# Performance work log

Hardware: AMD Instinct MI355X
Metric: run time of the kernel (lower is better)

Reference implementation:

```python
import jax, jax.numpy as jnp
from jax import lax
import numpy as np

N, W, H, C = 32, 64, 64, 256
D_STYLE = 256


def setup_inputs() -> dict:
    key = jax.random.key(0)
    k1, k2, k3, k4 = jax.random.split(key, 4)
    inputs = jax.random.normal(k1, (N, W, H, C), dtype=jnp.float32)
    style_coding = jax.random.normal(k2, (N, D_STYLE), dtype=jnp.float32)
    # he_normal-ish init scaling for the learned weights
    w_dense = jax.random.normal(k3, (D_STYLE, C), dtype=jnp.float32) * np.sqrt(2.0 / D_STYLE)
    w_conv = jax.random.normal(k4, (1, 1, C, C), dtype=jnp.float32) * np.sqrt(2.0 / C)
    return {"inputs": inputs, "style_coding": style_coding, "w_dense": w_dense, "w_conv": w_conv}


def reference(inputs, style_coding, w_dense, w_conv):
    # inputs: [N,W,H,C] (NHWC), style_coding: [N,D_style]
    c = inputs.shape[-1]
    scale = 1.0 / jnp.sqrt(jnp.float32(c))
    # Dense(fout_dim, use_bias=False, activation=LeakyReLU())  (keras default alpha=0.3)
    q = jax.nn.leaky_relu(style_coding @ w_dense, negative_slope=0.3)  # [N,C]
    # channel-wise attention: einsum('nwhc,nwhc->nc') with q broadcast over w,h
    ca_logits = jnp.einsum('nwhc,nc->nc', inputs, q) * scale           # [N,C]
    ca = jax.nn.softmax(ca_logits, axis=-1)[:, None, None, :]          # [N,1,1,C]
    # position-wise attention: einsum('nwhc,nwhc->nwh'), softmax over flattened W*H
    pa_logits = jnp.einsum('nwhc,nc->nwh', inputs, q) * scale          # [N,W,H]
    n, w, h = pa_logits.shape
    pa = jax.nn.softmax(pa_logits.reshape(n, w * h), axis=1).reshape(n, w, h, 1)
    x = inputs * ca * pa                                               # [N,W,H,C]
    # DarknetConv2D_BN_Leaky with no norm kwarg: 1x1 conv (no bias) + LeakyReLU(0.1)
    y = lax.conv_general_dilated(x, w_conv, window_strides=(1, 1), padding='SAME',
                                 dimension_numbers=('NHWC', 'HWIO', 'NHWC'))
    return jax.nn.leaky_relu(y, negative_slope=0.1)
```

## Files before the change

kernel.cpp:

```cpp
#include <hip/hip_runtime.h>


#define NBATCH 32
#define PIX 4096
#define CH 256
#define SCALE 0.0625f

typedef __attribute__((ext_vector_type(8))) short short8;
typedef __attribute__((ext_vector_type(4))) short short4v;
typedef __attribute__((ext_vector_type(4))) float floatx4;

__device__ __forceinline__ short f2bf(float x) {
    unsigned u = __builtin_bit_cast(unsigned, x);
    u += 0x7fffu + ((u >> 16) & 1u);
    return (short)(u >> 16);
}

__device__ __forceinline__ void gll16(const void* g, void* l) {
    __builtin_amdgcn_global_load_lds(
        (const __attribute__((address_space(1))) unsigned int*)g,
        (__attribute__((address_space(3))) unsigned int*)l, 16, 0, 0);
}

__global__ __launch_bounds__(256) void style_kernel(
    const float* __restrict__ style, const float* __restrict__ wd,
    float* __restrict__ q)
{
    __shared__ float s[256];
    const int n = blockIdx.x, t = threadIdx.x;
    s[t] = style[n * 256 + t];
    __syncthreads();
    float acc = 0.f;
#pragma unroll 8
    for (int k = 0; k < 256; ++k) acc += s[k] * wd[k * 256 + t];
    q[n * 256 + t] = acc > 0.f ? acc : 0.3f * acc;
}

__global__ __launch_bounds__(256) void reduce_cast_kernel(
    const float* __restrict__ inp, const float* __restrict__ q,
    float* __restrict__ colsum_part, float* __restrict__ pa_logits,
    short* __restrict__ bf16in)
{
    const int n = blockIdx.y;
    const int chunk = blockIdx.x;
    const int lane = threadIdx.x & 63, w = threadIdx.x >> 6;
    const float4 qv = *(const float4*)&q[n * 256 + lane * 4];
    float4 cs = make_float4(0.f, 0.f, 0.f, 0.f);
    const int pbase = chunk * 128 + w * 32;
    const float* base = inp + ((size_t)n * PIX + pbase) * CH;
    short* obase = bf16in + ((size_t)n * PIX + pbase) * CH;
    for (int j = 0; j < 32; ++j) {
        float4 v = *(const float4*)&base[(size_t)j * CH + lane * 4];
        float d = v.x * qv.x + v.y * qv.y + v.z * qv.z + v.w * qv.w;
        cs.x += v.x; cs.y += v.y; cs.z += v.z; cs.w += v.w;
        short4v sv;
        sv.x = f2bf(v.x); sv.y = f2bf(v.y); sv.z = f2bf(v.z); sv.w = f2bf(v.w);
        *(short4v*)&obase[(size_t)j * CH + lane * 4] = sv;
#pragma unroll
        for (int off = 32; off; off >>= 1) d += __shfl_xor(d, off);
        if (lane == 0) pa_logits[n * PIX + pbase + j] = d * SCALE;
    }
    *(float4*)&colsum_part[((size_t)n * 128 + chunk * 4 + w) * 256 + lane * 4] = cs;
}

__global__ __launch_bounds__(256) void softmax_kernel(
    const float* __restrict__ colsum_part, const float* __restrict__ q,
    const float* __restrict__ pa_logits,
    float* __restrict__ ca, float* __restrict__ pa)
{
    __shared__ float red[256];
    const int n = blockIdx.x, t = threadIdx.x;

    float csum = 0.f;
#pragma unroll 8
    for (int i = 0; i < 128; ++i) csum += colsum_part[((size_t)n * 128 + i) * 256 + t];
    float lg = csum * q[n * 256 + t] * SCALE;
    red[t] = lg; __syncthreads();
    for (int s = 128; s > 0; s >>= 1) {
        if (t < s) red[t] = fmaxf(red[t], red[t + s]);
        __syncthreads();
    }
    float m = red[0]; __syncthreads();
    float e = expf(lg - m);
    red[t] = e; __syncthreads();
    for (int s = 128; s > 0; s >>= 1) {
        if (t < s) red[t] += red[t + s];
        __syncthreads();
    }
    ca[n * 256 + t] = e / red[0];
    __syncthreads();

    float lv[16];
    float lmax = -1e30f;
#pragma unroll
    for (int i = 0; i < 16; ++i) {
        lv[i] = pa_logits[n * PIX + t + 256 * i];
        lmax = fmaxf(lmax, lv[i]);
    }
    red[t] = lmax; __syncthreads();
    for (int s = 128; s > 0; s >>= 1) {
        if (t < s) red[t] = fmaxf(red[t], red[t + s]);
        __syncthreads();
    }
    float M = red[0]; __syncthreads();
    float ev[16], lsum = 0.f;
#pragma unroll
    for (int i = 0; i < 16; ++i) { ev[i] = expf(lv[i] - M); lsum += ev[i]; }
    red[t] = lsum; __syncthreads();
    for (int s = 128; s > 0; s >>= 1) {
        if (t < s) red[t] += red[t + s];
        __syncthreads();
    }
    float inv = 1.0f / red[0];
#pragma unroll
    for (int i = 0; i < 16; ++i) pa[n * PIX + t + 256 * i] = ev[i] * inv;
}

__global__ void wscale_kernel(const float* __restrict__ wc,
                              const float* __restrict__ ca,
                              short* __restrict__ wscaled)
{
    __shared__ float tile[32][33];
    const int n = blockIdx.z;
    const int co0 = blockIdx.x * 32, ci0 = blockIdx.y * 32;
    const int tx = threadIdx.x, ty = threadIdx.y;
#pragma unroll
    for (int r = 0; r < 4; ++r)
        tile[ty + r * 8][tx] = wc[(ci0 + ty + r * 8) * 256 + co0 + tx];
    const float cav = ca[n * 256 + ci0 + tx];
    __syncthreads();
#pragma unroll
    for (int r = 0; r < 4; ++r)
        wscaled[(size_t)n * 65536 + (co0 + ty + r * 8) * 256 + ci0 + tx] =
            f2bf(tile[tx][ty + r * 8] * cav);
}

__global__ __launch_bounds__(256, 4) void conv_mfma(
    const short* __restrict__ bf16in, const short* __restrict__ wscaled,
    const float* __restrict__ pa, float* __restrict__ out)
{
    __shared__ __attribute__((aligned(16))) short As[64 * 64];
    __shared__ __attribute__((aligned(16))) short Bs[256 * 64];

    const int n  = blockIdx.y;
    const int m0 = blockIdx.x * 64;
    const int tid = threadIdx.x;
    const int lane = tid & 63, wid = tid >> 6;
    const int l16 = lane & 15, quad = lane >> 4;
    const int l8r = lane >> 3, slot = lane & 7;

    floatx4 acc[4][4] = {};

    const short* Agb = bf16in + ((size_t)n * PIX + m0) * CH;
    const short* Bgb = wscaled + (size_t)n * 65536;

    for (int kb = 0; kb < 4; ++kb) {
        const int k0 = kb * 64;
        if (kb) __syncthreads();
#pragma unroll
        for (int i = 0; i < 2; ++i) {
            const int r = wid * 16 + i * 8 + l8r;
            gll16(Agb + (size_t)r * CH + k0 + ((slot ^ (r & 7)) << 3),
                  &As[(wid * 16 + i * 8) * 64]);
        }
#pragma unroll
        for (int i = 0; i < 8; ++i) {
            const int c = wid * 64 + i * 8 + l8r;
            gll16(Bgb + (size_t)c * CH + k0 + ((slot ^ (c & 7)) << 3),
                  &Bs[(wid * 64 + i * 8) * 64]);
        }
        __syncthreads();
#pragma unroll
        for (int kk2 = 0; kk2 < 2; ++kk2) {
            const int sx = ((kk2 * 4 + quad) ^ (l16 & 7)) << 3;
            short8 af[4], bfr[4];
#pragma unroll
            for (int mt = 0; mt < 4; ++mt)
                af[mt] = *(const short8*)&As[(mt * 16 + l16) * 64 + sx];
#pragma unroll
            for (int nt = 0; nt < 4; ++nt)
                bfr[nt] = *(const short8*)&Bs[(wid * 64 + nt * 16 + l16) * 64 + sx];
#pragma unroll
            for (int mt = 0; mt < 4; ++mt)
#pragma unroll
                for (int nt = 0; nt < 4; ++nt)
                    acc[mt][nt] = __builtin_amdgcn_mfma_f32_16x16x32_bf16(
                        af[mt], bfr[nt], acc[mt][nt], 0, 0, 0);
        }
    }

#pragma unroll
    for (int mt = 0; mt < 4; ++mt) {
#pragma unroll
        for (int reg = 0; reg < 4; ++reg) {
            const int pix = m0 + mt * 16 + quad * 4 + reg;
            const float pav = pa[n * PIX + pix];
            float* orow = out + ((size_t)(n * PIX + pix)) * CH + wid * 64;
#pragma unroll
            for (int nt = 0; nt < 4; ++nt) {
                float z = acc[mt][nt][reg] * pav;
                orow[nt * 16 + l16] = z > 0.f ? z : 0.1f * z;
            }
        }
    }
}

extern "C" void kernel_launch(void* const* d_in, const int* in_sizes, int n_in,
                              void* d_out, int out_size, void* d_ws, size_t ws_size,
                              hipStream_t stream) {
    const float* inputs = (const float*)d_in[0];
    const float* style  = (const float*)d_in[1];
    const float* wdense = (const float*)d_in[2];
    const float* wconv  = (const float*)d_in[3];
    float* out = (float*)d_out;

    char* ws = (char*)d_ws;
    float* q           = (float*)(ws + 0);
    float* ca          = (float*)(ws + 32768);
    float* pa_logits   = (float*)(ws + 65536);
    float* pa          = (float*)(ws + 589824);
    float* colsum_part = (float*)(ws + 1114112);
    short* wscaled     = (short*)(ws + 5308416);
    short* bf16in      = (short*)(ws + 9502720);

    style_kernel<<<NBATCH, 256, 0, stream>>>(style, wdense, q);
    reduce_cast_kernel<<<dim3(32, NBATCH), 256, 0, stream>>>(inputs, q, colsum_part,
                                                             pa_logits, bf16in);
    softmax_kernel<<<NBATCH, 256, 0, stream>>>(colsum_part, q, pa_logits, ca, pa);
    wscale_kernel<<<dim3(8, 8, NBATCH), dim3(32, 8), 0, stream>>>(wconv, ca, wscaled);
    conv_mfma<<<dim3(64, NBATCH), 256, 0, stream>>>(bf16in, wscaled, pa, out);
}
```

Baseline: 316.5 us.

## Fuse style GEMV into reduce, wscale into softmax, double-buffer conv LDS

Each reduce block now recomputes the per-batch style projection q itself, which removes the separate style kernel. The weight scaling by channel attention moves into the softmax kernel, cutting the pipeline from five launches to three. The conv kernel gains double-buffered LDS staging so the next K tile loads while the current one computes, with occupancy lowered to 2 blocks per SM. The trade-offs are redundant GEMV work (32x per batch), a serialized wscale over only 32 blocks, and halved occupancy in the conv.

Result: no change. 316.3 us (-0.1%).

```diff
diff --git a/kernel.cpp b/kernel.cpp
--- a/kernel.cpp
+++ b/kernel.cpp
@@ -22,33 +22,33 @@
         (__attribute__((address_space(3))) unsigned int*)l, 16, 0, 0);
 }
 
-__global__ __launch_bounds__(256) void style_kernel(
-    const float* __restrict__ style, const float* __restrict__ wd,
-    float* __restrict__ q)
+__global__ __launch_bounds__(256) void reduce_cast_q(
+    const float* __restrict__ inp, const float* __restrict__ style,
+    const float* __restrict__ wd,
+    float* __restrict__ q_out, float* __restrict__ colsum_part,
+    float* __restrict__ pa_logits, short* __restrict__ bf16in)
 {
     __shared__ float s[256];
-    const int n = blockIdx.x, t = threadIdx.x;
+    __shared__ float q_s[256];
+    const int n = blockIdx.y, chunk = blockIdx.x, t = threadIdx.x;
+
     s[t] = style[n * 256 + t];
     __syncthreads();
     float acc = 0.f;
 #pragma unroll 8
     for (int k = 0; k < 256; ++k) acc += s[k] * wd[k * 256 + t];
-    q[n * 256 + t] = acc > 0.f ? acc : 0.3f * acc;
-}
-
-__global__ __launch_bounds__(256) void reduce_cast_kernel(
-    const float* __restrict__ inp, const float* __restrict__ q,
-    float* __restrict__ colsum_part, float* __restrict__ pa_logits,
-    short* __restrict__ bf16in)
-{
-    const int n = blockIdx.y;
-    const int chunk = blockIdx.x;
-    const int lane = threadIdx.x & 63, w = threadIdx.x >> 6;
-    const float4 qv = *(const float4*)&q[n * 256 + lane * 4];
+    acc = acc > 0.f ? acc : 0.3f * acc;
+    q_s[t] = acc;
+    if (chunk == 0) q_out[n * 256 + t] = acc;
+    __syncthreads();
+
+    const int lane = t & 63, w = t >> 6;
+    const float4 qv = *(const float4*)&q_s[lane * 4];
     float4 cs = make_float4(0.f, 0.f, 0.f, 0.f);
     const int pbase = chunk * 128 + w * 32;
     const float* base = inp + ((size_t)n * PIX + pbase) * CH;
     short* obase = bf16in + ((size_t)n * PIX + pbase) * CH;
+#pragma unroll 4
     for (int j = 0; j < 32; ++j) {
         float4 v = *(const float4*)&base[(size_t)j * CH + lane * 4];
         float d = v.x * qv.x + v.y * qv.y + v.z * qv.z + v.w * qv.w;
@@ -63,12 +63,14 @@
     *(float4*)&colsum_part[((size_t)n * 128 + chunk * 4 + w) * 256 + lane * 4] = cs;
 }
 
-__global__ __launch_bounds__(256) void softmax_kernel(
+__global__ __launch_bounds__(256) void softmax_wscale(
     const float* __restrict__ colsum_part, const float* __restrict__ q,
-    const float* __restrict__ pa_logits,
-    float* __restrict__ ca, float* __restrict__ pa)
+    const float* __restrict__ pa_logits, const float* __restrict__ wc,
+    float* __restrict__ pa, short* __restrict__ wscaled)
 {
     __shared__ float red[256];
+    __shared__ float ca_s[256];
+    __shared__ float wt[32][257];
     const int n = blockIdx.x, t = threadIdx.x;
 
     float csum = 0.f;
@@ -87,7 +89,7 @@
         if (t < s) red[t] += red[t + s];
         __syncthreads();
     }
-    ca[n * 256 + t] = e / red[0];
+    ca_s[t] = e / red[0];
     __syncthreads();
 
     float lv[16];
@@ -114,33 +116,38 @@
     float inv = 1.0f / red[0];
 #pragma unroll
     for (int i = 0; i < 16; ++i) pa[n * PIX + t + 256 * i] = ev[i] * inv;
-}
-
-__global__ void wscale_kernel(const float* __restrict__ wc,
-                              const float* __restrict__ ca,
-                              short* __restrict__ wscaled)
-{
-    __shared__ float tile[32][33];
-    const int n = blockIdx.z;
-    const int co0 = blockIdx.x * 32, ci0 = blockIdx.y * 32;
-    const int tx = threadIdx.x, ty = threadIdx.y;
-#pragma unroll
-    for (int r = 0; r < 4; ++r)
-        tile[ty + r * 8][tx] = wc[(ci0 + ty + r * 8) * 256 + co0 + tx];
-    const float cav = ca[n * 256 + ci0 + tx];
-    __syncthreads();
-#pragma unroll
-    for (int r = 0; r < 4; ++r)
-        wscaled[(size_t)n * 65536 + (co0 + ty + r * 8) * 256 + ci0 + tx] =
-            f2bf(tile[tx][ty + r * 8] * cav);
-}
-
-__global__ __launch_bounds__(256, 4) void conv_mfma(
+
+    const int tx = t & 31, ty = t >> 5;
+    for (int strip = 0; strip < 8; ++strip) {
+        const int ci0 = strip * 32;
+        __syncthreads();
+#pragma unroll
+        for (int r = 0; r < 4; ++r) {
+            const int ci = ty + r * 8;
+#pragma unroll
+            for (int cb = 0; cb < 8; ++cb)
+                wt[ci][cb * 32 + tx] = wc[(ci0 + ci) * 256 + cb * 32 + tx];
+        }
+        __syncthreads();
+        const float cav = ca_s[ci0 + tx];
+#pragma unroll
+        for (int r = 0; r < 4; ++r) {
+#pragma unroll
+            for (int cb = 0; cb < 8; ++cb) {
+                const int co = cb * 32 + ty + r * 8;
+                wscaled[(size_t)n * 65536 + co * 256 + ci0 + tx] =
+                    f2bf(wt[tx][co] * cav);
+            }
+        }
+    }
+}
+
+__global__ __launch_bounds__(256, 2) void conv_mfma(
     const short* __restrict__ bf16in, const short* __restrict__ wscaled,
     const float* __restrict__ pa, float* __restrict__ out)
 {
-    __shared__ __attribute__((aligned(16))) short As[64 * 64];
-    __shared__ __attribute__((aligned(16))) short Bs[256 * 64];
+    __shared__ __attribute__((aligned(16))) short As[2][64 * 64];
+    __shared__ __attribute__((aligned(16))) short Bs[2][256 * 64];
 
     const int n  = blockIdx.y;
     const int m0 = blockIdx.x * 64;
@@ -154,32 +161,38 @@
     const short* Agb = bf16in + ((size_t)n * PIX + m0) * CH;
     const short* Bgb = wscaled + (size_t)n * 65536;
 
-    for (int kb = 0; kb < 4; ++kb) {
+    auto stage = [&](int kb, int buf) {
         const int k0 = kb * 64;
-        if (kb) __syncthreads();
 #pragma unroll
         for (int i = 0; i < 2; ++i) {
             const int r = wid * 16 + i * 8 + l8r;
             gll16(Agb + (size_t)r * CH + k0 + ((slot ^ (r & 7)) << 3),
-                  &As[(wid * 16 + i * 8) * 64]);
+                  &As[buf][(wid * 16 + i * 8) * 64]);
         }
 #pragma unroll
         for (int i = 0; i < 8; ++i) {
             const int c = wid * 64 + i * 8 + l8r;
             gll16(Bgb + (size_t)c * CH + k0 + ((slot ^ (c & 7)) << 3),
-                  &Bs[(wid * 64 + i * 8) * 64]);
-        }
-        __syncthreads();
+                  &Bs[buf][(wid * 64 + i * 8) * 64]);
+        }
+    };
+
+    stage(0, 0);
+    __syncthreads();
+
+    for (int kb = 0; kb < 4; ++kb) {
+        const int cur = kb & 1;
+        if (kb < 3) stage(kb + 1, cur ^ 1);
 #pragma unroll
         for (int kk2 = 0; kk2 < 2; ++kk2) {
             const int sx = ((kk2 * 4 + quad) ^ (l16 & 7)) << 3;
             short8 af[4], bfr[4];
 #pragma unroll
             for (int mt = 0; mt < 4; ++mt)
-                af[mt] = *(const short8*)&As[(mt * 16 + l16) * 64 + sx];
+                af[mt] = *(const short8*)&As[cur][(mt * 16 + l16) * 64 + sx];
 #pragma unroll
             for (int nt = 0; nt < 4; ++nt)
-                bfr[nt] = *(const short8*)&Bs[(wid * 64 + nt * 16 + l16) * 64 + sx];
+                bfr[nt] = *(const short8*)&Bs[cur][(wid * 64 + nt * 16 + l16) * 64 + sx];
 #pragma unroll
             for (int mt = 0; mt < 4; ++mt)
 #pragma unroll
@@ -187,6 +200,7 @@
                     acc[mt][nt] = __builtin_amdgcn_mfma_f32_16x16x32_bf16(
                         af[mt], bfr[nt], acc[mt][nt], 0, 0, 0);
         }
+        __syncthreads();
     }
 
 #pragma unroll
@@ -216,17 +230,15 @@
 
     char* ws = (char*)d_ws;
     float* q           = (float*)(ws + 0);
-    float* ca          = (float*)(ws + 32768);
-    float* pa_logits   = (float*)(ws + 65536);
-    float* pa          = (float*)(ws + 589824);
-    float* colsum_part = (float*)(ws + 1114112);
-    short* wscaled     = (short*)(ws + 5308416);
-    short* bf16in      = (short*)(ws + 9502720);
-
-    style_kernel<<<NBATCH, 256, 0, stream>>>(style, wdense, q);
-    reduce_cast_kernel<<<dim3(32, NBATCH), 256, 0, stream>>>(inputs, q, colsum_part,
-                                                             pa_logits, bf16in);
-    softmax_kernel<<<NBATCH, 256, 0, stream>>>(colsum_part, q, pa_logits, ca, pa);
-    wscale_kernel<<<dim3(8, 8, NBATCH), dim3(32, 8), 0, stream>>>(wconv, ca, wscaled);
+    float* pa_logits   = (float*)(ws + 32768);
+    float* pa          = (float*)(ws + 557056);
+    float* colsum_part = (float*)(ws + 1081344);
+    short* wscaled     = (short*)(ws + 5275648);
+    short* bf16in      = (short*)(ws + 9469952);
+
+    reduce_cast_q<<<dim3(32, NBATCH), 256, 0, stream>>>(inputs, style, wdense, q,
+                                                        colsum_part, pa_logits, bf16in);
+    softmax_wscale<<<NBATCH, 256, 0, stream>>>(colsum_part, q, pa_logits, wconv,
+                                               pa, wscaled);
     conv_mfma<<<dim3(64, NBATCH), 256, 0, stream>>>(bf16in, wscaled, pa, out);
 }
```
